# Optimization experiments

Hardware: AMD Instinct MI355X
Metric: run time of the kernel (lower is better)

The kernel has to match this reference:

```python
import jax, jax.numpy as jnp
import numpy as np

N_NODES = 100000
N_EDGES = 6400000
IN_CH = 128
NEG_SLOPE = 0.2


def setup_inputs() -> dict:
    key = jax.random.key(0)
    k1, k2, k3, k4, k5 = jax.random.split(key, 5)
    x = jax.random.normal(k1, (N_NODES, IN_CH), dtype=jnp.float32)
    edge_index = jax.random.randint(k2, (2, N_EDGES), 0, N_NODES, dtype=jnp.int64)
    # GATConv params (heads=1, out_channels=1): glorot-style scale
    W = jax.random.normal(k3, (IN_CH, 1), dtype=jnp.float32) / np.sqrt(IN_CH)
    att_src = jax.random.normal(k4, (1,), dtype=jnp.float32)
    att_dst = jax.random.normal(k5, (1,), dtype=jnp.float32)
    bias = jnp.zeros((1,), dtype=jnp.float32)
    return {"x": x, "edge_index": edge_index, "W": W,
            "att_src": att_src, "att_dst": att_dst, "bias": bias}


def reference(x, edge_index, W, att_src, att_dst, bias):
    N = x.shape[0]
    h = (x @ W)[:, 0]                      # [N] projected features (out_channels=1)
    # add self-loops (PyG default add_self_loops=True)
    loop = jnp.arange(N, dtype=edge_index.dtype)
    src = jnp.concatenate([edge_index[0], loop])   # [E+N]
    dst = jnp.concatenate([edge_index[1], loop])
    a_s = h * att_src[0]                   # per-node src attention term
    a_d = h * att_dst[0]                   # per-node dst attention term
    logits = jax.nn.leaky_relu(a_s[src] + a_d[dst], NEG_SLOPE)  # [E+N]
    # segment softmax over incoming edges of each destination node
    seg_max = jax.ops.segment_max(logits, dst, num_segments=N)
    e = jnp.exp(logits - seg_max[dst])
    denom = jax.ops.segment_sum(e, dst, num_segments=N)
    alpha = e / (denom[dst] + 1e-16)
    # scatter-aggregate weighted source features
    out = jax.ops.segment_sum(alpha * h[src], dst, num_segments=N)  # [N]
    return out[:, None] + bias             # [N, 1]
```

## Files before the change

### kernel.cpp

```cpp
#include <hip/hip_runtime.h>

#define IN_CH 128
#define NEG_SLOPE 0.2f
#define BINSZ 8000
#define NBINS 13
#define NW 8192
#define MAX_SG 39
#define MAX_BPB 40
#define F_NUM 2097152.0f
#define F_DEN 16777216.0f
#define INV_F_NUM 4.76837158203125e-7f
#define INV_F_DEN 5.9604644775390625e-8f

typedef int   vi4 __attribute__((ext_vector_type(4)));
typedef float vf4 __attribute__((ext_vector_type(4)));

__device__ __forceinline__ float lrelu(float v) { return v > 0.f ? v : NEG_SLOPE * v; }
__device__ __forceinline__ unsigned enc_max(float f) {
    unsigned u = __float_as_uint(f);
    return (u & 0x80000000u) ? ~u : (u | 0x80000000u);
}
__device__ __forceinline__ float dec_max(unsigned e) {
    return (e & 0x80000000u) ? __uint_as_float(e ^ 0x80000000u) : __uint_as_float(~e);
}

__global__ __launch_bounds__(256)
void proj_kernel(const float* __restrict__ x, const float* __restrict__ W,
                 const float* __restrict__ att_dst,
                 float* __restrict__ h, float* __restrict__ ad_h, int n) {
    int gtid   = blockIdx.x * blockDim.x + threadIdx.x;
    int wid    = gtid >> 6;
    int lane   = threadIdx.x & 63;
    int nwaves = (gridDim.x * blockDim.x) >> 6;
    int half   = lane >> 5;
    int hl     = lane & 31;

    vf4 w4 = reinterpret_cast<const vf4*>(W)[hl];
    const float ad = att_dst[0];

    int npair = n >> 1;
    for (int p0 = wid * 4; p0 < npair; p0 += nwaves * 4) {
        float s[4];
        #pragma unroll
        for (int k = 0; k < 4; ++k) {
            int p = p0 + k;
            s[k] = 0.f;
            if (p < npair) {
                int row = 2 * p + half;
                vf4 v = __builtin_nontemporal_load(
                    reinterpret_cast<const vf4*>(x + (size_t)row * IN_CH) + hl);
                s[k] = v.x * w4.x + v.y * w4.y + v.z * w4.z + v.w * w4.w;
            }
        }
        #pragma unroll
        for (int k = 0; k < 4; ++k) {
            #pragma unroll
            for (int off = 16; off > 0; off >>= 1) s[k] += __shfl_xor(s[k], off);
        }
        #pragma unroll
        for (int k = 0; k < 4; ++k) {
            int p = p0 + k;
            if (p < npair && hl == 0) {
                int row = 2 * p + half;
                h[row] = s[k];
                ad_h[row] = s[k] * ad;
            }
        }
    }
    if ((n & 1) && wid == 0) {
        int row = n - 1;
        vf4 v = reinterpret_cast<const vf4*>(x + (size_t)row * IN_CH)[hl];
        float s = v.x * w4.x + v.y * w4.y + v.z * w4.z + v.w * w4.w;
        #pragma unroll
        for (int off = 16; off > 0; off >>= 1) s += __shfl_xor(s, off);
        if (lane == 0) { h[row] = s; ad_h[row] = s * ad; }
    }
}

__global__ __launch_bounds__(256)
void hmax_kernel(const float* __restrict__ h,
                 const float* __restrict__ att_src, const float* __restrict__ att_dst,
                 unsigned* __restrict__ maxenc, int n) {
    const float as = att_src[0];
    const float ad = att_dst[0];
    float m1 = -1e30f, m2 = -1e30f;
    for (int i = blockIdx.x * blockDim.x + threadIdx.x; i < n;
         i += gridDim.x * blockDim.x) {
        float v = h[i];
        m1 = fmaxf(m1, v * as);
        m2 = fmaxf(m2, v * ad);
    }
    #pragma unroll
    for (int off = 32; off > 0; off >>= 1) {
        m1 = fmaxf(m1, __shfl_xor(m1, off));
        m2 = fmaxf(m2, __shfl_xor(m2, off));
    }
    __shared__ float bm[2][4];
    int wv = threadIdx.x >> 6;
    if ((threadIdx.x & 63) == 0) { bm[0][wv] = m1; bm[1][wv] = m2; }
    __syncthreads();
    if (threadIdx.x == 0) {
        float a = fmaxf(fmaxf(bm[0][0], bm[0][1]), fmaxf(bm[0][2], bm[0][3]));
        float b = fmaxf(fmaxf(bm[1][0], bm[1][1]), fmaxf(bm[1][2], bm[1][3]));
        atomicMax(maxenc,     enc_max(a));
        atomicMax(maxenc + 1, enc_max(b));
    }
}

__global__ __launch_bounds__(256)
void count_kernel(const int* __restrict__ dst_idx, int* __restrict__ wc, int E) {
    int lane = threadIdx.x & 63, wv = threadIdx.x >> 6;
    int g = blockIdx.x * 4 + wv;
    long long E4 = E >> 2;
    long long e0 = 4 * (E4 * g / NW);
    long long e1 = (g == NW - 1) ? (long long)E : 4 * (E4 * (g + 1) / NW);

    int cnt = 0;
    for (long long i0 = e0; i0 < e1; i0 += 64) {
        long long i = i0 + lane;
        int b = NBINS;
        if (i < e1) b = __builtin_nontemporal_load(dst_idx + i) / BINSZ;
        #pragma unroll
        for (int b2 = 0; b2 < NBINS; ++b2) {
            unsigned long long m = __ballot(b == b2);
            if (lane == b2) cnt += __popcll(m);
        }
    }
    if (lane < NBINS) wc[lane * NW + g] = cnt;
}

__global__ __launch_bounds__(256)
void scanA_kernel(const int* __restrict__ wc, int* __restrict__ bsum) {
    __shared__ int wt[4];
    int t = threadIdx.x, lane = t & 63, wv = t >> 6;
    vi4 c = *reinterpret_cast<const vi4*>(wc + blockIdx.x * 1024 + 4 * t);
    int s = c.x + c.y + c.z + c.w;
    #pragma unroll
    for (int off = 32; off > 0; off >>= 1) s += __shfl_xor(s, off);
    if (lane == 0) wt[wv] = s;
    __syncthreads();
    if (t == 0) bsum[blockIdx.x] = wt[0] + wt[1] + wt[2] + wt[3];
}

__global__ __launch_bounds__(128)
void scanB_kernel(const int* __restrict__ bsum, int* __restrict__ bbase,
                  int* __restrict__ rbase, int* __restrict__ hist, int nchunk) {
    __shared__ int sb[129];
    __shared__ int wt[2];
    int t = threadIdx.x, lane = t & 63, wv = t >> 6;
    int v = (t < nchunk) ? bsum[t] : 0;
    int inc = v;
    #pragma unroll
    for (int d2 = 1; d2 < 64; d2 <<= 1) { int u = __shfl_up(inc, d2); if (lane >= d2) inc += u; }
    if (lane == 63) wt[wv] = inc;
    __syncthreads();
    int excl = ((wv == 1) ? wt[0] : 0) + inc - v;
    sb[t] = excl;
    if (t == 127) sb[128] = excl + v;
    __syncthreads();
    if (t < nchunk) bbase[t] = sb[t];
    if (t < NBINS) {
        int rb = sb[t * (NW / 1024)];
        rbase[t] = rb;
        int nb = (t == NBINS - 1) ? sb[128] : sb[(t + 1) * (NW / 1024)];
        hist[t] = nb - rb;
    }
}

__global__ __launch_bounds__(256)
void scanC_kernel(const int* __restrict__ wc, const int* __restrict__ bbase,
                  int* __restrict__ wbase) {
    __shared__ int wt[4];
    int t = threadIdx.x, lane = t & 63, wv = t >> 6;
    int base = blockIdx.x * 1024 + 4 * t;
    vi4 c = *reinterpret_cast<const vi4*>(wc + base);
    int s0 = c.x, s1 = s0 + c.y, s2 = s1 + c.z, s3 = s2 + c.w;
    int tot = s3;
    int inc = tot;
    #pragma unroll
    for (int d2 = 1; d2 < 64; d2 <<= 1) { int u = __shfl_up(inc, d2); if (lane >= d2) inc += u; }
    if (lane == 63) wt[wv] = inc;
    __syncthreads();
    int wb = 0;
    for (int k = 0; k < wv; ++k) wb += wt[k];
    int excl = bbase[blockIdx.x] + wb + inc - tot;
    vi4 o; o.x = excl; o.y = excl + s0; o.z = excl + s1; o.w = excl + s2;
    *reinterpret_cast<vi4*>(wbase + base) = o;
}

__global__ __launch_bounds__(256)
void place_kernel(const int* __restrict__ src_idx, const int* __restrict__ dst_idx,
                  const int* __restrict__ wbase, unsigned* __restrict__ rec, int E) {
    __shared__ int ccur[4][NBINS];
    int lane = threadIdx.x & 63, wv = threadIdx.x >> 6;
    int g = blockIdx.x * 4 + wv;
    if (lane < NBINS) ccur[wv][lane] = wbase[lane * NW + g];
    __syncthreads();

    long long E4 = E >> 2;
    long long e0 = 4 * (E4 * g / NW);
    long long e1 = (g == NW - 1) ? (long long)E : 4 * (E4 * (g + 1) / NW);
    for (long long i0 = e0; i0 < e1; i0 += 256) {
        long long i = i0 + 4 * lane;
        if (i < e1) {
            vi4 d4 = __builtin_nontemporal_load(reinterpret_cast<const vi4*>(dst_idx + i));
            vi4 s4 = __builtin_nontemporal_load(reinterpret_cast<const vi4*>(src_idx + i));
            int b0 = d4.x / BINSZ, b1 = d4.y / BINSZ, b2 = d4.z / BINSZ, b3 = d4.w / BINSZ;
            int p0 = atomicAdd(&ccur[wv][b0], 1);
            int p1 = atomicAdd(&ccur[wv][b1], 1);
            int p2 = atomicAdd(&ccur[wv][b2], 1);
            int p3 = atomicAdd(&ccur[wv][b3], 1);
            rec[p0] = ((unsigned)(d4.x - b0 * BINSZ) << 17) | (unsigned)s4.x;
            rec[p1] = ((unsigned)(d4.y - b1 * BINSZ) << 17) | (unsigned)s4.y;
            rec[p2] = ((unsigned)(d4.z - b2 * BINSZ) << 17) | (unsigned)s4.z;
            rec[p3] = ((unsigned)(d4.w - b3 * BINSZ) << 17) | (unsigned)s4.w;
        }
    }
}

__global__ __launch_bounds__(1024)
void gather_kernel(const unsigned* __restrict__ rec,
                   const float* __restrict__ h, const float* __restrict__ ad_h,
                   const float* __restrict__ att_src, const unsigned* __restrict__ maxenc,
                   const int* __restrict__ rbase, const int* __restrict__ hist,
                   unsigned long long* __restrict__ part, int SG) {
    __shared__ __align__(16) unsigned long long s_acc[BINSZ];

    int bin   = blockIdx.x / SG;
    int slice = blockIdx.x - bin * SG;
    long long r0 = rbase[bin];
    int cnt   = hist[bin];
    long long g0 = r0 + (long long)cnt * slice / SG;
    long long g1 = r0 + (long long)cnt * (slice + 1) / SG;

    {
        vi4 z = {0, 0, 0, 0};
        for (int k = threadIdx.x; k < BINSZ / 2; k += 1024)
            *reinterpret_cast<vi4*>(&s_acc[2 * k]) = z;
    }
    __syncthreads();

    const float as = att_src[0];
    const float L  = lrelu(dec_max(maxenc[0]) + dec_max(maxenc[1]));
    const float* adw = ad_h + bin * BINSZ;

    auto process1 = [&](unsigned q) {
        int s0 = q & 0x1FFFFu, ri = q >> 17;
        float h0 = h[s0];
        float e0 = __expf(lrelu(fmaf(h0, as, adw[ri])) - L);
        unsigned long long p0 = ((unsigned long long)(long long)__float2int_rn(e0 * h0 * F_NUM) << 32)
                              + __float2uint_rn(e0 * F_DEN);
        atomicAdd(&s_acc[ri], p0);
    };

    long long a0 = (g0 + 3) & ~3LL;
    long long a1 = g1 & ~3LL;
    long long headEnd, tail0;
    if (a0 <= a1) { headEnd = a0; tail0 = a1; }
    else          { headEnd = g1; tail0 = g1; a0 = 0; a1 = 0; }

    for (long long i = g0 + threadIdx.x; i < headEnd; i += 1024) process1(rec[i]);

    long long i = a0 + 4 * (long long)threadIdx.x;
    vi4 q;
    bool have = (i < a1);
    if (have) q = __builtin_nontemporal_load(reinterpret_cast<const vi4*>(rec + i));
    while (have) {
        long long nx = i + 4096;
        bool nhave = (nx < a1);
        vi4 nq;
        if (nhave) nq = __builtin_nontemporal_load(reinterpret_cast<const vi4*>(rec + nx));
        unsigned q0 = (unsigned)q.x, q1 = (unsigned)q.y, q2 = (unsigned)q.z, q3 = (unsigned)q.w;
        int s0 = q0 & 0x1FFFFu, r0i = q0 >> 17;
        int s1 = q1 & 0x1FFFFu, r1i = q1 >> 17;
        int s2 = q2 & 0x1FFFFu, r2i = q2 >> 17;
        int s3 = q3 & 0x1FFFFu, r3i = q3 >> 17;
        float h0 = h[s0], h1 = h[s1], h2 = h[s2], h3 = h[s3];
        float a0f = adw[r0i], a1f = adw[r1i], a2f = adw[r2i], a3f = adw[r3i];
        float e0 = __expf(lrelu(fmaf(h0, as, a0f)) - L);
        float e1 = __expf(lrelu(fmaf(h1, as, a1f)) - L);
        float e2 = __expf(lrelu(fmaf(h2, as, a2f)) - L);
        float e3 = __expf(lrelu(fmaf(h3, as, a3f)) - L);
        unsigned long long p0 = ((unsigned long long)(long long)__float2int_rn(e0 * h0 * F_NUM) << 32) + __float2uint_rn(e0 * F_DEN);
        unsigned long long p1 = ((unsigned long long)(long long)__float2int_rn(e1 * h1 * F_NUM) << 32) + __float2uint_rn(e1 * F_DEN);
        unsigned long long p2 = ((unsigned long long)(long long)__float2int_rn(e2 * h2 * F_NUM) << 32) + __float2uint_rn(e2 * F_DEN);
        unsigned long long p3 = ((unsigned long long)(long long)__float2int_rn(e3 * h3 * F_NUM) << 32) + __float2uint_rn(e3 * F_DEN);
        atomicAdd(&s_acc[r0i], p0);
        atomicAdd(&s_acc[r1i], p1);
        atomicAdd(&s_acc[r2i], p2);
        atomicAdd(&s_acc[r3i], p3);
        i = nx; q = nq; have = nhave;
    }

    for (long long i2 = tail0 + threadIdx.x; i2 < g1; i2 += 1024) process1(rec[i2]);
    __syncthreads();

    unsigned long long* outp = part + (size_t)blockIdx.x * BINSZ;
    for (int k = threadIdx.x; k < BINSZ / 2; k += 1024) {
        vi4 v = *reinterpret_cast<const vi4*>(&s_acc[2 * k]);
        __builtin_nontemporal_store(v, reinterpret_cast<vi4*>(outp + 2 * k));
    }
}

__global__ void reduce_final(const unsigned long long* __restrict__ part,
                             const float* __restrict__ h,
                             const float* __restrict__ att_src, const float* __restrict__ att_dst,
                             const float* __restrict__ bias, const unsigned* __restrict__ maxenc,
                             float* __restrict__ out, int n, int SG) {
    int i = blockIdx.x * blockDim.x + threadIdx.x;
    if (i >= n) return;
    int bin = i / BINSZ;
    int off = i - bin * BINSZ;
    float num = 0.f, den = 0.f;
    const unsigned long long* p = part + (size_t)(bin * SG) * BINSZ;
    for (int s = 0; s < SG; ++s) {
        unsigned long long v = __builtin_nontemporal_load(p + off);
        num += (float)(int)(v >> 32);
        den += (float)(unsigned)(v & 0xffffffffULL);
        p += BINSZ;
    }
    num *= INV_F_NUM;
    den *= INV_F_DEN;
    const float L = lrelu(dec_max(maxenc[0]) + dec_max(maxenc[1]));
    float hv = h[i];
    float e  = __expf(lrelu(hv * (att_src[0] + att_dst[0])) - L);
    out[i] = (num + e * hv) / (den + e + 1e-30f) + bias[0];
}

__global__ __launch_bounds__(1024)
void binpass_kernel(const int* __restrict__ src_idx, const int* __restrict__ dst_idx,
                    const float* __restrict__ h,
                    const float* __restrict__ att_src, const float* __restrict__ att_dst,
                    float* __restrict__ part, int E, int n, int BPB) {
    __shared__ float s_num[BINSZ];
    __shared__ float s_den[BINSZ];

    int bin   = blockIdx.x / BPB;
    int slice = blockIdx.x - bin * BPB;
    int base  = bin * BINSZ;
    int blen  = min(BINSZ, n - base);

    for (int k = threadIdx.x; k < BINSZ; k += 1024) { s_num[k] = 0.f; s_den[k] = 0.f; }
    __syncthreads();

    const float as = att_src[0];
    const float ad = att_dst[0];

    long long e0 = (long long)E * slice / BPB;
    long long e1 = (long long)E * (slice + 1) / BPB;
    for (long long i = e0 + threadIdx.x; i < e1; i += 1024) {
        int d = dst_idx[i];
        unsigned r = (unsigned)(d - base);
        if (r < (unsigned)blen) {
            int s = src_idx[i];
            float hs = h[s];
            float v  = fmaf(hs, as, h[d] * ad);
            float e  = __expf(lrelu(v));
            atomicAdd(&s_num[r], e * hs);
            atomicAdd(&s_den[r], e);
        }
    }
    __syncthreads();

    float* outp = part + (size_t)blockIdx.x * (2 * BINSZ);
    for (int k = threadIdx.x; k < BINSZ; k += 1024) {
        outp[k]         = s_num[k];
        outp[BINSZ + k] = s_den[k];
    }
}

__global__ void fb_reduce_final(const float* __restrict__ part, const float* __restrict__ h,
                                const float* __restrict__ att_src, const float* __restrict__ att_dst,
                                const float* __restrict__ bias, float* __restrict__ out,
                                int n, int BPB) {
    int i = blockIdx.x * blockDim.x + threadIdx.x;
    if (i >= n) return;
    int bin = i / BINSZ;
    int off = i - bin * BINSZ;
    float num = 0.f, den = 0.f;
    const float* p = part + (size_t)(bin * BPB) * (2 * BINSZ);
    for (int s = 0; s < BPB; ++s) {
        num += p[off];
        den += p[BINSZ + off];
        p += 2 * BINSZ;
    }
    float hv = h[i];
    float e  = __expf(lrelu(hv * (att_src[0] + att_dst[0])));
    out[i] = (num + e * hv) / (den + e + 1e-16f) + bias[0];
}

__global__ void edge_kernel(const int* __restrict__ src_idx, const int* __restrict__ dst_idx,
                            const float* __restrict__ h,
                            const float* __restrict__ att_src, const float* __restrict__ att_dst,
                            float* __restrict__ nd, int E) {
    const float as = att_src[0];
    const float ad = att_dst[0];
    int i      = blockIdx.x * blockDim.x + threadIdx.x;
    int stride = gridDim.x * blockDim.x;
    for (; i < E; i += stride) {
        int s = src_idx[i];
        int d = dst_idx[i];
        float hs = h[s];
        float e  = __expf(lrelu(fmaf(hs, as, h[d] * ad)));
        unsafeAtomicAdd(&nd[2 * d],     e * hs);
        unsafeAtomicAdd(&nd[2 * d + 1], e);
    }
}

__global__ void final_kernel(const float* __restrict__ h, const float* __restrict__ nd,
                             const float* __restrict__ att_src, const float* __restrict__ att_dst,
                             const float* __restrict__ bias, float* __restrict__ out, int n) {
    int i = blockIdx.x * blockDim.x + threadIdx.x;
    if (i >= n) return;
    float hv = h[i];
    float e  = __expf(lrelu(hv * (att_src[0] + att_dst[0])));
    out[i] = (nd[2 * i] + e * hv) / (nd[2 * i + 1] + e + 1e-16f) + bias[0];
}

extern "C" void kernel_launch(void* const* d_in, const int* in_sizes, int n_in,
                              void* d_out, int out_size, void* d_ws, size_t ws_size,
                              hipStream_t stream) {
    const float* x       = (const float*)d_in[0];
    const int*   ei      = (const int*)d_in[1];
    const float* W       = (const float*)d_in[2];
    const float* att_src = (const float*)d_in[3];
    const float* att_dst = (const float*)d_in[4];
    const float* bias    = (const float*)d_in[5];
    float*       out     = (float*)d_out;

    const int n = out_size;
    const int E = in_sizes[1] / 2;

    const int NELEM  = NBINS * NW;
    const int NCHUNK = NELEM / 1024;

    size_t off = 0;
    auto alloc = [&](size_t bytes) { size_t p = off; off = (off + bytes + 255) & ~(size_t)255; return p; };
    size_t o_h    = alloc((size_t)n * sizeof(float));
    size_t o_adh  = alloc((size_t)n * sizeof(float));
    size_t o_wc   = alloc((size_t)NELEM * sizeof(int));
    size_t o_wb   = alloc((size_t)NELEM * sizeof(int));
    size_t o_bs   = alloc((size_t)NCHUNK * sizeof(int));
    size_t o_bb   = alloc((size_t)NCHUNK * sizeof(int));
    size_t o_meta = alloc(64 * sizeof(int));
    size_t o_rec  = alloc((size_t)E * sizeof(unsigned));
    size_t fixed  = off;

    float*    h      = (float*)((char*)d_ws + o_h);
    float*    ad_h   = (float*)((char*)d_ws + o_adh);
    int*      rbase  = (int*)((char*)d_ws + o_meta);
    int*      hist   = rbase + 16;
    unsigned* maxenc = (unsigned*)(rbase + 32);
    const size_t per = (size_t)BINSZ * sizeof(unsigned long long);

    int SG = 0;
    if (ws_size > fixed) SG = (int)((ws_size - fixed) / ((size_t)NBINS * per));
    if (SG > MAX_SG) SG = MAX_SG;

    bool ok_shape = (n <= NBINS * BINSZ) && ((E & 3) == 0) && (E >= 4 * NW);

    if (SG >= 8 && ok_shape) {
        int*                wc   = (int*)((char*)d_ws + o_wc);
        int*                wb   = (int*)((char*)d_ws + o_wb);
        int*                bsum = (int*)((char*)d_ws + o_bs);
        int*                bbase= (int*)((char*)d_ws + o_bb);
        unsigned*           rec  = (unsigned*)((char*)d_ws + o_rec);
        unsigned long long* part = (unsigned long long*)((char*)d_ws + fixed);

        hipMemsetAsync(maxenc, 0, 2 * sizeof(unsigned), stream);
        count_kernel<<<NW / 4, 256, 0, stream>>>(ei + E, wc, E);
        scanA_kernel<<<NCHUNK, 256, 0, stream>>>(wc, bsum);
        scanB_kernel<<<1, 128, 0, stream>>>(bsum, bbase, rbase, hist, NCHUNK);
        scanC_kernel<<<NCHUNK, 256, 0, stream>>>(wc, bbase, wb);
        place_kernel<<<NW / 4, 256, 0, stream>>>(ei, ei + E, wb, rec, E);
        proj_kernel<<<1024, 256, 0, stream>>>(x, W, att_dst, h, ad_h, n);
        hmax_kernel<<<120, 256, 0, stream>>>(h, att_src, att_dst, maxenc, n);
        gather_kernel<<<NBINS * SG, 1024, 0, stream>>>(rec, h, ad_h, att_src, maxenc,
                                                       rbase, hist, part, SG);
        reduce_final<<<(n + 255) / 256, 256, 0, stream>>>(part, h, att_src, att_dst,
                                                          bias, maxenc, out, n, SG);
    } else {
        proj_kernel<<<1024, 256, 0, stream>>>(x, W, att_dst, h, ad_h, n);
        size_t hb = (((size_t)n * 2 * sizeof(float)) + 255) & ~(size_t)255;
        int BPB = 0;
        if (ws_size > hb) BPB = (int)((ws_size - hb) / ((size_t)NBINS * per));
        if (BPB > MAX_BPB) BPB = MAX_BPB;

        if (BPB >= 6 && n <= NBINS * BINSZ) {
            float* part = (float*)((char*)d_ws + hb);
            binpass_kernel<<<NBINS * BPB, 1024, 0, stream>>>(
                ei, ei + E, h, att_src, att_dst, part, E, n, BPB);
            fb_reduce_final<<<(n + 255) / 256, 256, 0, stream>>>(
                part, h, att_src, att_dst, bias, out, n, BPB);
        } else {
            float* nd = (float*)((char*)d_ws + hb);
            hipMemsetAsync(nd, 0, (size_t)n * 2 * sizeof(float), stream);
            edge_kernel<<<2048, 256, 0, stream>>>(ei, ei + E, h, att_src, att_dst, nd, E);
            final_kernel<<<(n + 255) / 256, 256, 0, stream>>>(h, nd, att_src, att_dst,
                                                              bias, out, n);
        }
    }
}
```

Baseline: 138.1 us.

## Fuse projection into placement kernel, use ballot-based binning, software-pipeline gather

```diff
diff --git a/kernel.cpp b/kernel.cpp
--- a/kernel.cpp
+++ b/kernel.cpp
@@ -24,16 +24,13 @@
     return (e & 0x80000000u) ? __uint_as_float(e ^ 0x80000000u) : __uint_as_float(~e);
 }
 
-__global__ __launch_bounds__(256)
-void proj_kernel(const float* __restrict__ x, const float* __restrict__ W,
-                 const float* __restrict__ att_dst,
-                 float* __restrict__ h, float* __restrict__ ad_h, int n) {
-    int gtid   = blockIdx.x * blockDim.x + threadIdx.x;
-    int wid    = gtid >> 6;
-    int lane   = threadIdx.x & 63;
-    int nwaves = (gridDim.x * blockDim.x) >> 6;
-    int half   = lane >> 5;
-    int hl     = lane & 31;
+__device__ __forceinline__ void do_proj(const float* __restrict__ x, const float* __restrict__ W,
+                                        const float* __restrict__ att_dst,
+                                        float* __restrict__ h, float* __restrict__ ad_h,
+                                        int n, int wid, int nwaves) {
+    int lane = threadIdx.x & 63;
+    int half = lane >> 5;
+    int hl   = lane & 31;
 
     vf4 w4 = reinterpret_cast<const vf4*>(W)[hl];
     const float ad = att_dst[0];
@@ -78,6 +75,15 @@
 }
 
 __global__ __launch_bounds__(256)
+void proj_kernel(const float* __restrict__ x, const float* __restrict__ W,
+                 const float* __restrict__ att_dst,
+                 float* __restrict__ h, float* __restrict__ ad_h, int n) {
+    int wid    = (blockIdx.x * blockDim.x + threadIdx.x) >> 6;
+    int nwaves = (gridDim.x * blockDim.x) >> 6;
+    do_proj(x, W, att_dst, h, ad_h, n, wid, nwaves);
+}
+
+__global__ __launch_bounds__(256)
 void hmax_kernel(const float* __restrict__ h,
                  const float* __restrict__ att_src, const float* __restrict__ att_dst,
                  unsigned* __restrict__ maxenc, int n) {
@@ -189,32 +195,45 @@
 }
 
 __global__ __launch_bounds__(256)
-void place_kernel(const int* __restrict__ src_idx, const int* __restrict__ dst_idx,
-                  const int* __restrict__ wbase, unsigned* __restrict__ rec, int E) {
-    __shared__ int ccur[4][NBINS];
+void place_proj_kernel(const int* __restrict__ src_idx, const int* __restrict__ dst_idx,
+                       const int* __restrict__ wbase, unsigned* __restrict__ rec, int E,
+                       const float* __restrict__ x, const float* __restrict__ W,
+                       const float* __restrict__ att_dst,
+                       float* __restrict__ h, float* __restrict__ ad_h, int n) {
+    int b = blockIdx.x;
+    int role = b % 3;
+    if (role == 2) {
+        int qid = b / 3;
+        int wid = qid * 4 + (threadIdx.x >> 6);
+        do_proj(x, W, att_dst, h, ad_h, n, wid, 4096);
+        return;
+    }
+    int pid  = (b / 3) * 2 + role;
     int lane = threadIdx.x & 63, wv = threadIdx.x >> 6;
-    int g = blockIdx.x * 4 + wv;
-    if (lane < NBINS) ccur[wv][lane] = wbase[lane * NW + g];
-    __syncthreads();
-
+    int g = pid * 4 + wv;
     long long E4 = E >> 2;
     long long e0 = 4 * (E4 * g / NW);
     long long e1 = (g == NW - 1) ? (long long)E : 4 * (E4 * (g + 1) / NW);
-    for (long long i0 = e0; i0 < e1; i0 += 256) {
-        long long i = i0 + 4 * lane;
-        if (i < e1) {
-            vi4 d4 = __builtin_nontemporal_load(reinterpret_cast<const vi4*>(dst_idx + i));
-            vi4 s4 = __builtin_nontemporal_load(reinterpret_cast<const vi4*>(src_idx + i));
-            int b0 = d4.x / BINSZ, b1 = d4.y / BINSZ, b2 = d4.z / BINSZ, b3 = d4.w / BINSZ;
-            int p0 = atomicAdd(&ccur[wv][b0], 1);
-            int p1 = atomicAdd(&ccur[wv][b1], 1);
-            int p2 = atomicAdd(&ccur[wv][b2], 1);
-            int p3 = atomicAdd(&ccur[wv][b3], 1);
-            rec[p0] = ((unsigned)(d4.x - b0 * BINSZ) << 17) | (unsigned)s4.x;
-            rec[p1] = ((unsigned)(d4.y - b1 * BINSZ) << 17) | (unsigned)s4.y;
-            rec[p2] = ((unsigned)(d4.z - b2 * BINSZ) << 17) | (unsigned)s4.z;
-            rec[p3] = ((unsigned)(d4.w - b3 * BINSZ) << 17) | (unsigned)s4.w;
-        }
+
+    unsigned long long ltmask = (1ULL << lane) - 1;
+    int cur = (lane < NBINS) ? wbase[lane * NW + g] : 0;
+
+    for (long long i0 = e0; i0 < e1; i0 += 64) {
+        long long i = i0 + lane;
+        bool valid = (i < e1);
+        int d = valid ? __builtin_nontemporal_load(dst_idx + i) : 0;
+        int s = valid ? __builtin_nontemporal_load(src_idx + i) : 0;
+        int bb = valid ? d / BINSZ : NBINS;
+        int r  = d - (d / BINSZ) * BINSZ;
+        int pos = 0;
+        #pragma unroll
+        for (int b2 = 0; b2 < NBINS; ++b2) {
+            unsigned long long m = __ballot(bb == b2);
+            int base_b = __shfl(cur, b2);
+            if (bb == b2) pos = base_b + __popcll(m & ltmask);
+            if (lane == b2) cur += __popcll(m);
+        }
+        if (valid) rec[pos] = ((unsigned)r << 17) | (unsigned)s;
     }
 }
 
@@ -261,35 +280,61 @@
 
     for (long long i = g0 + threadIdx.x; i < headEnd; i += 1024) process1(rec[i]);
 
-    long long i = a0 + 4 * (long long)threadIdx.x;
-    vi4 q;
-    bool have = (i < a1);
-    if (have) q = __builtin_nontemporal_load(reinterpret_cast<const vi4*>(rec + i));
-    while (have) {
-        long long nx = i + 4096;
-        bool nhave = (nx < a1);
-        vi4 nq;
-        if (nhave) nq = __builtin_nontemporal_load(reinterpret_cast<const vi4*>(rec + nx));
-        unsigned q0 = (unsigned)q.x, q1 = (unsigned)q.y, q2 = (unsigned)q.z, q3 = (unsigned)q.w;
-        int s0 = q0 & 0x1FFFFu, r0i = q0 >> 17;
-        int s1 = q1 & 0x1FFFFu, r1i = q1 >> 17;
-        int s2 = q2 & 0x1FFFFu, r2i = q2 >> 17;
-        int s3 = q3 & 0x1FFFFu, r3i = q3 >> 17;
-        float h0 = h[s0], h1 = h[s1], h2 = h[s2], h3 = h[s3];
-        float a0f = adw[r0i], a1f = adw[r1i], a2f = adw[r2i], a3f = adw[r3i];
-        float e0 = __expf(lrelu(fmaf(h0, as, a0f)) - L);
-        float e1 = __expf(lrelu(fmaf(h1, as, a1f)) - L);
-        float e2 = __expf(lrelu(fmaf(h2, as, a2f)) - L);
-        float e3 = __expf(lrelu(fmaf(h3, as, a3f)) - L);
-        unsigned long long p0 = ((unsigned long long)(long long)__float2int_rn(e0 * h0 * F_NUM) << 32) + __float2uint_rn(e0 * F_DEN);
-        unsigned long long p1 = ((unsigned long long)(long long)__float2int_rn(e1 * h1 * F_NUM) << 32) + __float2uint_rn(e1 * F_DEN);
-        unsigned long long p2 = ((unsigned long long)(long long)__float2int_rn(e2 * h2 * F_NUM) << 32) + __float2uint_rn(e2 * F_DEN);
-        unsigned long long p3 = ((unsigned long long)(long long)__float2int_rn(e3 * h3 * F_NUM) << 32) + __float2uint_rn(e3 * F_DEN);
-        atomicAdd(&s_acc[r0i], p0);
-        atomicAdd(&s_acc[r1i], p1);
-        atomicAdd(&s_acc[r2i], p2);
-        atomicAdd(&s_acc[r3i], p3);
-        i = nx; q = nq; have = nhave;
+    const long long step = 4096;
+    long long iA = a0 + 4 * (long long)threadIdx.x;
+    bool vA = (iA < a1);
+    vi4 qA = {0,0,0,0};
+    if (vA) qA = __builtin_nontemporal_load(reinterpret_cast<const vi4*>(rec + iA));
+
+    long long iB = iA + step;
+    bool vB = (iB < a1);
+    vi4 qB = {0,0,0,0};
+    if (vB) qB = __builtin_nontemporal_load(reinterpret_cast<const vi4*>(rec + iB));
+
+    int   rA0=0, rA1=0, rA2=0, rA3=0;
+    float hA0=0, hA1=0, hA2=0, hA3=0, dA0=0, dA1=0, dA2=0, dA3=0;
+    if (vA) {
+        unsigned u0=(unsigned)qA.x, u1=(unsigned)qA.y, u2=(unsigned)qA.z, u3=(unsigned)qA.w;
+        int sA0=u0&0x1FFFFu, sA1=u1&0x1FFFFu, sA2=u2&0x1FFFFu, sA3=u3&0x1FFFFu;
+        rA0=u0>>17; rA1=u1>>17; rA2=u2>>17; rA3=u3>>17;
+        hA0=h[sA0]; hA1=h[sA1]; hA2=h[sA2]; hA3=h[sA3];
+        dA0=adw[rA0]; dA1=adw[rA1]; dA2=adw[rA2]; dA3=adw[rA3];
+    }
+
+    while (vA) {
+        long long iC = iB + step;
+        bool vC = (iC < a1);
+        vi4 qC = {0,0,0,0};
+        if (vC) qC = __builtin_nontemporal_load(reinterpret_cast<const vi4*>(rec + iC));
+
+        int   rB0=0, rB1=0, rB2=0, rB3=0;
+        float hB0=0, hB1=0, hB2=0, hB3=0, dB0=0, dB1=0, dB2=0, dB3=0;
+        if (vB) {
+            unsigned u0=(unsigned)qB.x, u1=(unsigned)qB.y, u2=(unsigned)qB.z, u3=(unsigned)qB.w;
+            int sB0=u0&0x1FFFFu, sB1=u1&0x1FFFFu, sB2=u2&0x1FFFFu, sB3=u3&0x1FFFFu;
+            rB0=u0>>17; rB1=u1>>17; rB2=u2>>17; rB3=u3>>17;
+            hB0=h[sB0]; hB1=h[sB1]; hB2=h[sB2]; hB3=h[sB3];
+            dB0=adw[rB0]; dB1=adw[rB1]; dB2=adw[rB2]; dB3=adw[rB3];
+        }
+
+        float e0 = __expf(lrelu(fmaf(hA0, as, dA0)) - L);
+        float e1 = __expf(lrelu(fmaf(hA1, as, dA1)) - L);
+        float e2 = __expf(lrelu(fmaf(hA2, as, dA2)) - L);
+        float e3 = __expf(lrelu(fmaf(hA3, as, dA3)) - L);
+        unsigned long long p0 = ((unsigned long long)(long long)__float2int_rn(e0 * hA0 * F_NUM) << 32) + __float2uint_rn(e0 * F_DEN);
+        unsigned long long p1 = ((unsigned long long)(long long)__float2int_rn(e1 * hA1 * F_NUM) << 32) + __float2uint_rn(e1 * F_DEN);
+        unsigned long long p2 = ((unsigned long long)(long long)__float2int_rn(e2 * hA2 * F_NUM) << 32) + __float2uint_rn(e2 * F_DEN);
+        unsigned long long p3 = ((unsigned long long)(long long)__float2int_rn(e3 * hA3 * F_NUM) << 32) + __float2uint_rn(e3 * F_DEN);
+        atomicAdd(&s_acc[rA0], p0);
+        atomicAdd(&s_acc[rA1], p1);
+        atomicAdd(&s_acc[rA2], p2);
+        atomicAdd(&s_acc[rA3], p3);
+
+        vA = vB;
+        rA0=rB0; rA1=rB1; rA2=rB2; rA3=rB3;
+        hA0=hB0; hA1=hB1; hA2=hB2; hA3=hB3;
+        dA0=dB0; dA1=dB1; dA2=dB2; dA3=dB3;
+        vB = vC; qB = qC; iB = iC;
     }
 
     for (long long i2 = tail0 + threadIdx.x; i2 < g1; i2 += 1024) process1(rec[i2]);
@@ -457,7 +502,7 @@
     if (ws_size > fixed) SG = (int)((ws_size - fixed) / ((size_t)NBINS * per));
     if (SG > MAX_SG) SG = MAX_SG;
 
-    bool ok_shape = (n <= NBINS * BINSZ) && ((E & 3) == 0) && (E >= 4 * NW);
+    bool ok_shape = (n <= NBINS * BINSZ) && ((E & 3) == 0) && (E >= 4 * NW) && ((n & 1) == 0);
 
     if (SG >= 8 && ok_shape) {
         int*                wc   = (int*)((char*)d_ws + o_wc);
@@ -472,8 +517,8 @@
         scanA_kernel<<<NCHUNK, 256, 0, stream>>>(wc, bsum);
         scanB_kernel<<<1, 128, 0, stream>>>(bsum, bbase, rbase, hist, NCHUNK);
         scanC_kernel<<<NCHUNK, 256, 0, stream>>>(wc, bbase, wb);
-        place_kernel<<<NW / 4, 256, 0, stream>>>(ei, ei + E, wb, rec, E);
-        proj_kernel<<<1024, 256, 0, stream>>>(x, W, att_dst, h, ad_h, n);
+        place_proj_kernel<<<3072, 256, 0, stream>>>(ei, ei + E, wb, rec, E,
+                                                    x, W, att_dst, h, ad_h, n);
         hmax_kernel<<<120, 256, 0, stream>>>(h, att_src, att_dst, maxenc, n);
         gather_kernel<<<NBINS * SG, 1024, 0, stream>>>(rec, h, ad_h, att_src, maxenc,
                                                        rbase, hist, part, SG);
```

After: 144.5 us. 1.05x slower.

## Fuse projection into count kernel and pack bf16 source feature into edge records

Applied to the files above, without the earlier changes.

```diff
diff --git a/kernel.cpp b/kernel.cpp
--- a/kernel.cpp
+++ b/kernel.cpp
@@ -23,17 +23,18 @@
 __device__ __forceinline__ float dec_max(unsigned e) {
     return (e & 0x80000000u) ? __uint_as_float(e ^ 0x80000000u) : __uint_as_float(~e);
 }
-
-__global__ __launch_bounds__(256)
-void proj_kernel(const float* __restrict__ x, const float* __restrict__ W,
-                 const float* __restrict__ att_dst,
-                 float* __restrict__ h, float* __restrict__ ad_h, int n) {
-    int gtid   = blockIdx.x * blockDim.x + threadIdx.x;
-    int wid    = gtid >> 6;
-    int lane   = threadIdx.x & 63;
-    int nwaves = (gridDim.x * blockDim.x) >> 6;
-    int half   = lane >> 5;
-    int hl     = lane & 31;
+__device__ __forceinline__ unsigned bf16_rne(float f) {
+    unsigned u = __float_as_uint(f);
+    return (u + 0x7FFFu + ((u >> 16) & 1u)) >> 16;
+}
+
+__device__ __forceinline__ void do_proj(const float* __restrict__ x, const float* __restrict__ W,
+                                        const float* __restrict__ att_dst,
+                                        float* __restrict__ h, float* __restrict__ ad_h,
+                                        int n, int wid, int nwaves) {
+    int lane = threadIdx.x & 63;
+    int half = lane >> 5;
+    int hl   = lane & 31;
 
     vf4 w4 = reinterpret_cast<const vf4*>(W)[hl];
     const float ad = att_dst[0];
@@ -78,6 +79,49 @@
 }
 
 __global__ __launch_bounds__(256)
+void proj_kernel(const float* __restrict__ x, const float* __restrict__ W,
+                 const float* __restrict__ att_dst,
+                 float* __restrict__ h, float* __restrict__ ad_h, int n) {
+    int wid    = (blockIdx.x * blockDim.x + threadIdx.x) >> 6;
+    int nwaves = (gridDim.x * blockDim.x) >> 6;
+    do_proj(x, W, att_dst, h, ad_h, n, wid, nwaves);
+}
+
+__global__ __launch_bounds__(256)
+void count_proj_kernel(const int* __restrict__ dst_idx, int* __restrict__ wc, int E,
+                       const float* __restrict__ x, const float* __restrict__ W,
+                       const float* __restrict__ att_dst,
+                       float* __restrict__ h, float* __restrict__ ad_h, int n) {
+    int b = blockIdx.x;
+    int role = b % 3;
+    if (role == 2) {
+        int qid = b / 3;
+        int wid = qid * 4 + (threadIdx.x >> 6);
+        do_proj(x, W, att_dst, h, ad_h, n, wid, 4096);
+        return;
+    }
+    int pid  = (b / 3) * 2 + role;
+    int lane = threadIdx.x & 63, wv = threadIdx.x >> 6;
+    int g = pid * 4 + wv;
+    long long E4 = E >> 2;
+    long long e0 = 4 * (E4 * g / NW);
+    long long e1 = (g == NW - 1) ? (long long)E : 4 * (E4 * (g + 1) / NW);
+
+    int cnt = 0;
+    for (long long i0 = e0; i0 < e1; i0 += 64) {
+        long long i = i0 + lane;
+        int bb = NBINS;
+        if (i < e1) bb = __builtin_nontemporal_load(dst_idx + i) / BINSZ;
+        #pragma unroll
+        for (int b2 = 0; b2 < NBINS; ++b2) {
+            unsigned long long m = __ballot(bb == b2);
+            if (lane == b2) cnt += __popcll(m);
+        }
+    }
+    if (lane < NBINS) wc[lane * NW + g] = cnt;
+}
+
+__global__ __launch_bounds__(256)
 void hmax_kernel(const float* __restrict__ h,
                  const float* __restrict__ att_src, const float* __restrict__ att_dst,
                  unsigned* __restrict__ maxenc, int n) {
@@ -105,28 +149,6 @@
         atomicMax(maxenc,     enc_max(a));
         atomicMax(maxenc + 1, enc_max(b));
     }
-}
-
-__global__ __launch_bounds__(256)
-void count_kernel(const int* __restrict__ dst_idx, int* __restrict__ wc, int E) {
-    int lane = threadIdx.x & 63, wv = threadIdx.x >> 6;
-    int g = blockIdx.x * 4 + wv;
-    long long E4 = E >> 2;
-    long long e0 = 4 * (E4 * g / NW);
-    long long e1 = (g == NW - 1) ? (long long)E : 4 * (E4 * (g + 1) / NW);
-
-    int cnt = 0;
-    for (long long i0 = e0; i0 < e1; i0 += 64) {
-        long long i = i0 + lane;
-        int b = NBINS;
-        if (i < e1) b = __builtin_nontemporal_load(dst_idx + i) / BINSZ;
-        #pragma unroll
-        for (int b2 = 0; b2 < NBINS; ++b2) {
-            unsigned long long m = __ballot(b == b2);
-            if (lane == b2) cnt += __popcll(m);
-        }
-    }
-    if (lane < NBINS) wc[lane * NW + g] = cnt;
 }
 
 __global__ __launch_bounds__(256)
@@ -190,6 +212,7 @@
 
 __global__ __launch_bounds__(256)
 void place_kernel(const int* __restrict__ src_idx, const int* __restrict__ dst_idx,
+                  const float* __restrict__ h,
                   const int* __restrict__ wbase, unsigned* __restrict__ rec, int E) {
     __shared__ int ccur[4][NBINS];
     int lane = threadIdx.x & 63, wv = threadIdx.x >> 6;
@@ -205,22 +228,23 @@
         if (i < e1) {
             vi4 d4 = __builtin_nontemporal_load(reinterpret_cast<const vi4*>(dst_idx + i));
             vi4 s4 = __builtin_nontemporal_load(reinterpret_cast<const vi4*>(src_idx + i));
+            float h0 = h[s4.x], h1 = h[s4.y], h2 = h[s4.z], h3 = h[s4.w];
             int b0 = d4.x / BINSZ, b1 = d4.y / BINSZ, b2 = d4.z / BINSZ, b3 = d4.w / BINSZ;
             int p0 = atomicAdd(&ccur[wv][b0], 1);
             int p1 = atomicAdd(&ccur[wv][b1], 1);
             int p2 = atomicAdd(&ccur[wv][b2], 1);
             int p3 = atomicAdd(&ccur[wv][b3], 1);
-            rec[p0] = ((unsigned)(d4.x - b0 * BINSZ) << 17) | (unsigned)s4.x;
-            rec[p1] = ((unsigned)(d4.y - b1 * BINSZ) << 17) | (unsigned)s4.y;
-            rec[p2] = ((unsigned)(d4.z - b2 * BINSZ) << 17) | (unsigned)s4.z;
-            rec[p3] = ((unsigned)(d4.w - b3 * BINSZ) << 17) | (unsigned)s4.w;
+            rec[p0] = ((unsigned)(d4.x - b0 * BINSZ) << 16) | bf16_rne(h0);
+            rec[p1] = ((unsigned)(d4.y - b1 * BINSZ) << 16) | bf16_rne(h1);
+            rec[p2] = ((unsigned)(d4.z - b2 * BINSZ) << 16) | bf16_rne(h2);
+            rec[p3] = ((unsigned)(d4.w - b3 * BINSZ) << 16) | bf16_rne(h3);
         }
     }
 }
 
 __global__ __launch_bounds__(1024)
 void gather_kernel(const unsigned* __restrict__ rec,
-                   const float* __restrict__ h, const float* __restrict__ ad_h,
+                   const float* __restrict__ ad_h,
                    const float* __restrict__ att_src, const unsigned* __restrict__ maxenc,
                    const int* __restrict__ rbase, const int* __restrict__ hist,
                    unsigned long long* __restrict__ part, int SG) {
@@ -245,8 +269,8 @@
     const float* adw = ad_h + bin * BINSZ;
 
     auto process1 = [&](unsigned q) {
-        int s0 = q & 0x1FFFFu, ri = q >> 17;
-        float h0 = h[s0];
+        int ri = q >> 16;
+        float h0 = __uint_as_float(q << 16);
         float e0 = __expf(lrelu(fmaf(h0, as, adw[ri])) - L);
         unsigned long long p0 = ((unsigned long long)(long long)__float2int_rn(e0 * h0 * F_NUM) << 32)
                               + __float2uint_rn(e0 * F_DEN);
@@ -262,25 +286,22 @@
     for (long long i = g0 + threadIdx.x; i < headEnd; i += 1024) process1(rec[i]);
 
     long long i = a0 + 4 * (long long)threadIdx.x;
-    vi4 q;
+    vi4 q = {0,0,0,0};
     bool have = (i < a1);
     if (have) q = __builtin_nontemporal_load(reinterpret_cast<const vi4*>(rec + i));
     while (have) {
         long long nx = i + 4096;
         bool nhave = (nx < a1);
-        vi4 nq;
+        vi4 nq = {0,0,0,0};
         if (nhave) nq = __builtin_nontemporal_load(reinterpret_cast<const vi4*>(rec + nx));
-        unsigned q0 = (unsigned)q.x, q1 = (unsigned)q.y, q2 = (unsigned)q.z, q3 = (unsigned)q.w;
-        int s0 = q0 & 0x1FFFFu, r0i = q0 >> 17;
-        int s1 = q1 & 0x1FFFFu, r1i = q1 >> 17;
-        int s2 = q2 & 0x1FFFFu, r2i = q2 >> 17;
-        int s3 = q3 & 0x1FFFFu, r3i = q3 >> 17;
-        float h0 = h[s0], h1 = h[s1], h2 = h[s2], h3 = h[s3];
-        float a0f = adw[r0i], a1f = adw[r1i], a2f = adw[r2i], a3f = adw[r3i];
-        float e0 = __expf(lrelu(fmaf(h0, as, a0f)) - L);
-        float e1 = __expf(lrelu(fmaf(h1, as, a1f)) - L);
-        float e2 = __expf(lrelu(fmaf(h2, as, a2f)) - L);
-        float e3 = __expf(lrelu(fmaf(h3, as, a3f)) - L);
+        unsigned u0=(unsigned)q.x, u1=(unsigned)q.y, u2=(unsigned)q.z, u3=(unsigned)q.w;
+        int r0i=u0>>16, r1i=u1>>16, r2i=u2>>16, r3i=u3>>16;
+        float h0=__uint_as_float(u0<<16), h1=__uint_as_float(u1<<16);
+        float h2=__uint_as_float(u2<<16), h3=__uint_as_float(u3<<16);
+        float e0 = __expf(lrelu(fmaf(h0, as, adw[r0i])) - L);
+        float e1 = __expf(lrelu(fmaf(h1, as, adw[r1i])) - L);
+        float e2 = __expf(lrelu(fmaf(h2, as, adw[r2i])) - L);
+        float e3 = __expf(lrelu(fmaf(h3, as, adw[r3i])) - L);
         unsigned long long p0 = ((unsigned long long)(long long)__float2int_rn(e0 * h0 * F_NUM) << 32) + __float2uint_rn(e0 * F_DEN);
         unsigned long long p1 = ((unsigned long long)(long long)__float2int_rn(e1 * h1 * F_NUM) << 32) + __float2uint_rn(e1 * F_DEN);
         unsigned long long p2 = ((unsigned long long)(long long)__float2int_rn(e2 * h2 * F_NUM) << 32) + __float2uint_rn(e2 * F_DEN);
@@ -457,7 +478,7 @@
     if (ws_size > fixed) SG = (int)((ws_size - fixed) / ((size_t)NBINS * per));
     if (SG > MAX_SG) SG = MAX_SG;
 
-    bool ok_shape = (n <= NBINS * BINSZ) && ((E & 3) == 0) && (E >= 4 * NW);
+    bool ok_shape = (n <= NBINS * BINSZ) && ((E & 3) == 0) && (E >= 4 * NW) && ((n & 1) == 0);
 
     if (SG >= 8 && ok_shape) {
         int*                wc   = (int*)((char*)d_ws + o_wc);
@@ -468,14 +489,14 @@
         unsigned long long* part = (unsigned long long*)((char*)d_ws + fixed);
 
         hipMemsetAsync(maxenc, 0, 2 * sizeof(unsigned), stream);
-        count_kernel<<<NW / 4, 256, 0, stream>>>(ei + E, wc, E);
+        count_proj_kernel<<<3072, 256, 0, stream>>>(ei + E, wc, E,
+                                                    x, W, att_dst, h, ad_h, n);
         scanA_kernel<<<NCHUNK, 256, 0, stream>>>(wc, bsum);
         scanB_kernel<<<1, 128, 0, stream>>>(bsum, bbase, rbase, hist, NCHUNK);
         scanC_kernel<<<NCHUNK, 256, 0, stream>>>(wc, bbase, wb);
-        place_kernel<<<NW / 4, 256, 0, stream>>>(ei, ei + E, wb, rec, E);
-        proj_kernel<<<1024, 256, 0, stream>>>(x, W, att_dst, h, ad_h, n);
+        place_kernel<<<NW / 4, 256, 0, stream>>>(ei, ei + E, h, wb, rec, E);
         hmax_kernel<<<120, 256, 0, stream>>>(h, att_src, att_dst, maxenc, n);
-        gather_kernel<<<NBINS * SG, 1024, 0, stream>>>(rec, h, ad_h, att_src, maxenc,
+        gather_kernel<<<NBINS * SG, 1024, 0, stream>>>(rec, ad_h, att_src, maxenc,
                                                        rbase, hist, part, SG);
         reduce_final<<<(n + 255) / 256, 256, 0, stream>>>(part, h, att_src, att_dst,
                                                           bias, maxenc, out, n, SG);
```

New measurement: 134.1 us. 1.03x faster.
